# Performance work log

Hardware: AMD Instinct MI355X
Metric: run time of the kernel (lower is better)

## Reference

```python
import jax, jax.numpy as jnp
import numpy as np

N = 12288
E = N * 32  # avg degree 32


def spmm(row, col, w, support):
    # out[i] = sum_{e: row[e]==i} w[e] * support[col[e]]
    return jax.ops.segment_sum(w[:, None] * support[col], row, num_segments=N)


def setup_inputs() -> dict:
    key = jax.random.key(0)
    ks = jax.random.split(key, 7)
    x = jax.random.normal(ks[0], (N, 512), dtype=jnp.float32)
    edge_row = jax.random.randint(ks[1], (E,), 0, N, dtype=jnp.int32)
    edge_col = jax.random.randint(ks[2], (E,), 0, N, dtype=jnp.int32)
    # row-normalized-ish positive edge weights
    edge_w = jax.random.uniform(ks[3], (E,), dtype=jnp.float32) / 32.0
    def xavier(k, fan_in, fan_out):
        bound = float(np.sqrt(6.0 / (fan_in + fan_out)))
        return jax.random.uniform(k, (fan_in, fan_out), jnp.float32, -bound, bound)
    W1 = xavier(ks[4], 512, 256)
    W2 = xavier(ks[5], 256, 128)
    W3 = xavier(ks[6], 128, 64)
    return {"x": x, "edge_row": edge_row, "edge_col": edge_col,
            "edge_w": edge_w, "W1": W1, "W2": W2, "W3": W3}


def reference(x, edge_row, edge_col, edge_w, W1, W2, W3):
    # GNNLayer 1 (active=True): tanh(x @ W) then spmm(adj, .)
    z1 = spmm(edge_row, edge_col, edge_w, jnp.tanh(x @ W1))
    # GNNLayer 2 (active=True)
    z2 = spmm(edge_row, edge_col, edge_w, jnp.tanh(z1 @ W2))
    # GNNLayer 3 (active=False): no activation
    z_igae = spmm(edge_row, edge_col, edge_w, z2 @ W3)  # [N, 64]
    # reconstructed adjacency: sigmoid(z z^T), [N, N]
    z_igae_adj = jax.nn.sigmoid(z_igae @ z_igae.T)
    return (z_igae, z_igae_adj)
```

## Files before the change

kernel.cpp:

```cpp
#include <hip/hip_runtime.h>
#include <hip/hip_bf16.h>

#define NNODES 12288
#define NEDGES (NNODES * 32)
#define ELLCAP 128

typedef __attribute__((ext_vector_type(4))) float f32x4;
typedef __attribute__((ext_vector_type(8))) __bf16 bf16x8;

__global__ __launch_bounds__(256) void prep_kernel(const float* __restrict__ W1,
                                                   const float* __restrict__ W2,
                                                   const float* __restrict__ W3,
                                                   __bf16* __restrict__ W1t,
                                                   __bf16* __restrict__ W2t,
                                                   __bf16* __restrict__ W3t,
                                                   int* __restrict__ deg) {
    int i = blockIdx.x * 256 + threadIdx.x;
    if (i < NNODES) { deg[i] = 0; return; }
    int j = i - NNODES;
    if (j < 512 * 256) { W1t[(size_t)(j % 256) * 512 + j / 256] = (__bf16)W1[j]; return; }
    j -= 512 * 256;
    if (j < 256 * 128) { W2t[(size_t)(j % 128) * 256 + j / 128] = (__bf16)W2[j]; return; }
    j -= 256 * 128;
    if (j < 128 * 64) { W3t[(size_t)(j % 64) * 128 + j / 64] = (__bf16)W3[j]; return; }
}

__global__ __launch_bounds__(256) void gemm1_scatter(const float* __restrict__ x,
                                                     const __bf16* __restrict__ W1t,
                                                     __bf16* __restrict__ h1,
                                                     const int* __restrict__ erow,
                                                     const int* __restrict__ ecol,
                                                     const float* __restrict__ ew,
                                                     int* __restrict__ deg,
                                                     int2* __restrict__ ell) {
    if (blockIdx.x >= 384) {
        int e = (blockIdx.x - 384) * 256 + threadIdx.x;
        int r = erow[e];
        int p = atomicAdd(&deg[r], 1);
        int2 cw; cw.x = ecol[e]; cw.y = __float_as_int(ew[e]);
        ell[(size_t)r * ELLCAP + p] = cw;
        return;
    }
    constexpr int K = 512, Nc = 256;
    int wave = threadIdx.x >> 6, lane = threadIdx.x & 63;
    int lr = lane & 15, kg = lane >> 4;
    int m0 = (blockIdx.x % 96) * 128 + wave * 32;
    int n0 = (blockIdx.x / 96) * 64;
    f32x4 acc[2][4];
#pragma unroll
    for (int mi = 0; mi < 2; mi++)
#pragma unroll
        for (int ni = 0; ni < 4; ni++) acc[mi][ni] = (f32x4){0.f, 0.f, 0.f, 0.f};
#pragma unroll
    for (int k0 = 0; k0 < K; k0 += 32) {
        bf16x8 af[2], bf[4];
#pragma unroll
        for (int mi = 0; mi < 2; mi++) {
            const float* ap = x + (size_t)(m0 + mi * 16 + lr) * K + k0 + kg * 8;
            f32x4 a0 = *(const f32x4*)ap;
            f32x4 a1 = *(const f32x4*)(ap + 4);
#pragma unroll
            for (int j = 0; j < 4; j++) { af[mi][j] = (__bf16)a0[j]; af[mi][4 + j] = (__bf16)a1[j]; }
        }
#pragma unroll
        for (int ni = 0; ni < 4; ni++)
            bf[ni] = *(const bf16x8*)(W1t + (size_t)(n0 + ni * 16 + lr) * K + k0 + kg * 8);
#pragma unroll
        for (int mi = 0; mi < 2; mi++)
#pragma unroll
            for (int ni = 0; ni < 4; ni++)
                acc[mi][ni] = __builtin_amdgcn_mfma_f32_16x16x32_bf16(af[mi], bf[ni], acc[mi][ni], 0, 0, 0);
    }
#pragma unroll
    for (int mi = 0; mi < 2; mi++)
#pragma unroll
        for (int ni = 0; ni < 4; ni++) {
            int col = n0 + ni * 16 + lr;
            int rowb = m0 + mi * 16 + kg * 4;
#pragma unroll
            for (int r = 0; r < 4; r++)
                h1[(size_t)(rowb + r) * Nc + col] = (__bf16)tanhf(acc[mi][ni][r]);
        }
}

template <bool TANH, int K>
__global__ __launch_bounds__(256) void gemm_mfma(const __bf16* __restrict__ A,
                                                 const __bf16* __restrict__ Wt,
                                                 __bf16* __restrict__ C, int Nc) {
    int wave = threadIdx.x >> 6, lane = threadIdx.x & 63;
    int lr = lane & 15, kg = lane >> 4;
    int m0 = blockIdx.x * 128 + wave * 32;
    int n0 = blockIdx.y * 64;
    f32x4 acc[2][4];
#pragma unroll
    for (int mi = 0; mi < 2; mi++)
#pragma unroll
        for (int ni = 0; ni < 4; ni++) acc[mi][ni] = (f32x4){0.f, 0.f, 0.f, 0.f};
#pragma unroll
    for (int k0 = 0; k0 < K; k0 += 32) {
        bf16x8 af[2], bf[4];
#pragma unroll
        for (int mi = 0; mi < 2; mi++)
            af[mi] = *(const bf16x8*)(A + (size_t)(m0 + mi * 16 + lr) * K + k0 + kg * 8);
#pragma unroll
        for (int ni = 0; ni < 4; ni++)
            bf[ni] = *(const bf16x8*)(Wt + (size_t)(n0 + ni * 16 + lr) * K + k0 + kg * 8);
#pragma unroll
        for (int mi = 0; mi < 2; mi++)
#pragma unroll
            for (int ni = 0; ni < 4; ni++)
                acc[mi][ni] = __builtin_amdgcn_mfma_f32_16x16x32_bf16(af[mi], bf[ni], acc[mi][ni], 0, 0, 0);
    }
#pragma unroll
    for (int mi = 0; mi < 2; mi++)
#pragma unroll
        for (int ni = 0; ni < 4; ni++) {
            int col = n0 + ni * 16 + lr;
            int rowb = m0 + mi * 16 + kg * 4;
#pragma unroll
            for (int r = 0; r < 4; r++) {
                float v = acc[mi][ni][r];
                if (TANH) v = tanhf(v);
                C[(size_t)(rowb + r) * Nc + col] = (__bf16)v;
            }
        }
}

__global__ __launch_bounds__(256) void fused_spmm_tanh_gemm(const int* __restrict__ deg,
                                                            const int2* __restrict__ ell,
                                                            const __bf16* __restrict__ g1,
                                                            const __bf16* __restrict__ W3t,
                                                            __bf16* __restrict__ g2) {
    constexpr int K = 128, NOUT = 64, L = K / 8;
    __shared__ __bf16 zs[16][K + 4];
    int tid = threadIdx.x;
    int rloc = tid / L;
    int f8 = (tid % L) * 8;
    int rglob = blockIdx.x * 16 + rloc;
    int d = deg[rglob];
    const int2* er = ell + (size_t)rglob * ELLCAP;
    float acc[8] = {};
#pragma unroll 8
    for (int e = 0; e < d; e++) {
        int2 cw = er[e];
        float w = __int_as_float(cw.y);
        bf16x8 hv = *(const bf16x8*)(g1 + (size_t)cw.x * K + f8);
#pragma unroll
        for (int j = 0; j < 8; j++) acc[j] = fmaf(w, (float)hv[j], acc[j]);
    }
    bf16x8 o;
#pragma unroll
    for (int j = 0; j < 8; j++) o[j] = (__bf16)tanhf(acc[j]);
    *(bf16x8*)&zs[rloc][f8] = o;
    __syncthreads();
    int wave = tid >> 6, lane = tid & 63;
    int lr = lane & 15, kg = lane >> 4;
    f32x4 c = (f32x4){0.f, 0.f, 0.f, 0.f};
#pragma unroll
    for (int ks = 0; ks < K / 32; ks++) {
        bf16x8 a = *(const bf16x8*)&zs[lr][ks * 32 + kg * 8];
        bf16x8 b = *(const bf16x8*)(W3t + (size_t)(wave * 16 + lr) * K + ks * 32 + kg * 8);
        c = __builtin_amdgcn_mfma_f32_16x16x32_bf16(a, b, c, 0, 0, 0);
    }
#pragma unroll
    for (int r = 0; r < 4; r++)
        g2[(size_t)(blockIdx.x * 16 + kg * 4 + r) * NOUT + wave * 16 + lr] = (__bf16)c[r];
}

__global__ __launch_bounds__(256) void spmm64(const int* __restrict__ deg,
                                              const int2* __restrict__ ell,
                                              const __bf16* __restrict__ h,
                                              __bf16* __restrict__ z) {
    int r = blockIdx.x * 32 + threadIdx.x / 8;
    int f8 = (threadIdx.x & 7) * 8;
    int d = deg[r];
    const int2* er = ell + (size_t)r * ELLCAP;
    float acc[8] = {};
#pragma unroll 8
    for (int e = 0; e < d; e++) {
        int2 cw = er[e];
        float w = __int_as_float(cw.y);
        bf16x8 hv = *(const bf16x8*)(h + (size_t)cw.x * 64 + f8);
#pragma unroll
        for (int j = 0; j < 8; j++) acc[j] = fmaf(w, (float)hv[j], acc[j]);
    }
    bf16x8 o;
#pragma unroll
    for (int j = 0; j < 8; j++) o[j] = (__bf16)acc[j];
    *(bf16x8*)(z + (size_t)r * 64 + f8) = o;
}

__global__ __launch_bounds__(256) void spmm_final(const int* __restrict__ deg,
                                                  const int2* __restrict__ ell,
                                                  const __bf16* __restrict__ h,
                                                  __bf16* __restrict__ z,
                                                  float* __restrict__ zf) {
    int r = blockIdx.x * 32 + threadIdx.x / 8;
    int f8 = (threadIdx.x & 7) * 8;
    int d = deg[r];
    const int2* er = ell + (size_t)r * ELLCAP;
    float acc[8] = {};
#pragma unroll 8
    for (int e = 0; e < d; e++) {
        int2 cw = er[e];
        float w = __int_as_float(cw.y);
        bf16x8 hv = *(const bf16x8*)(h + (size_t)cw.x * 64 + f8);
#pragma unroll
        for (int j = 0; j < 8; j++) acc[j] = fmaf(w, (float)hv[j], acc[j]);
    }
    bf16x8 o;
#pragma unroll
    for (int j = 0; j < 8; j++) o[j] = (__bf16)acc[j];
    *(bf16x8*)(z + (size_t)r * 64 + f8) = o;
    f32x4 o0, o1;
#pragma unroll
    for (int j = 0; j < 4; j++) { o0[j] = acc[j]; o1[j] = acc[4 + j]; }
    *(f32x4*)(zf + (size_t)r * 64 + f8) = o0;
    *(f32x4*)(zf + (size_t)r * 64 + f8 + 4) = o1;
}

__global__ __launch_bounds__(256) void zzt_sigmoid(const __bf16* __restrict__ Z,
                                                   float* __restrict__ out) {
    __shared__ float tile[2][16][260];
    int wave = threadIdx.x >> 6;
    int lane = threadIdx.x & 63;
    int lr = lane & 15;
    int kg = lane >> 4;
    int r0 = blockIdx.y * 64;
    int c0blk = blockIdx.x * 256;
    int c0 = c0blk + wave * 64;
    bf16x8 af[4][2], bfr[4][2];
#pragma unroll
    for (int i = 0; i < 4; i++)
#pragma unroll
        for (int ks = 0; ks < 2; ks++) {
            af[i][ks]  = *(const bf16x8*)(Z + (size_t)(r0 + i * 16 + lr) * 64 + ks * 32 + kg * 8);
            bfr[i][ks] = *(const bf16x8*)(Z + (size_t)(c0 + i * 16 + lr) * 64 + ks * 32 + kg * 8);
        }
    f32x4 acc[4][4];
#pragma unroll
    for (int mi = 0; mi < 4; mi++)
#pragma unroll
        for (int ni = 0; ni < 4; ni++) acc[mi][ni] = (f32x4){0.f, 0.f, 0.f, 0.f};
#pragma unroll
    for (int mi = 0; mi < 4; mi++)
#pragma unroll
        for (int ni = 0; ni < 4; ni++) {
            acc[mi][ni] = __builtin_amdgcn_mfma_f32_16x16x32_bf16(af[mi][0], bfr[ni][0], acc[mi][ni], 0, 0, 0);
            acc[mi][ni] = __builtin_amdgcn_mfma_f32_16x16x32_bf16(af[mi][1], bfr[ni][1], acc[mi][ni], 0, 0, 0);
        }
#pragma unroll
    for (int ni = 0; ni < 4; ni++) {
        int colb = wave * 64 + ni * 16 + lr;
#pragma unroll
        for (int r = 0; r < 4; r++) {
            float e = __expf(-acc[0][ni][r]);
            tile[0][kg * 4 + r][colb] = __builtin_amdgcn_rcpf(1.f + e);
        }
    }
    __syncthreads();
#pragma unroll
    for (int p = 0; p < 4; p++) {
        if (p < 3) {
#pragma unroll
            for (int ni = 0; ni < 4; ni++) {
                int colb = wave * 64 + ni * 16 + lr;
#pragma unroll
                for (int r = 0; r < 4; r++) {
                    float e = __expf(-acc[p + 1][ni][r]);
                    tile[(p + 1) & 1][kg * 4 + r][colb] = __builtin_amdgcn_rcpf(1.f + e);
                }
            }
        }
#pragma unroll
        for (int it = 0; it < 4; it++) {
            int rowl = it * 4 + wave;
            size_t grow = (size_t)(r0 + p * 16 + rowl);
            *(f32x4*)(out + grow * NNODES + c0blk + lane * 4) = *(const f32x4*)&tile[p & 1][rowl][lane * 4];
        }
        __syncthreads();
    }
}

extern "C" void kernel_launch(void* const* d_in, const int* in_sizes, int n_in,
                              void* d_out, int out_size, void* d_ws, size_t ws_size,
                              hipStream_t stream) {
    (void)in_sizes; (void)n_in; (void)out_size; (void)ws_size;
    const float* x  = (const float*)d_in[0];
    const int* erow = (const int*)d_in[1];
    const int* ecol = (const int*)d_in[2];
    const float* ew = (const float*)d_in[3];
    const float* W1 = (const float*)d_in[4];
    const float* W2 = (const float*)d_in[5];
    const float* W3 = (const float*)d_in[6];
    float* z_igae = (float*)d_out;
    float* adj = (float*)d_out + (size_t)NNODES * 64;

    char* ws = (char*)d_ws;
    size_t off = 0;
    auto alloc = [&](size_t bytes) {
        void* p = ws + off;
        off += (bytes + 255) & ~(size_t)255;
        return p;
    };
    __bf16* W1t = (__bf16*)alloc((size_t)512 * 256 * 2);
    __bf16* W2t = (__bf16*)alloc((size_t)256 * 128 * 2);
    __bf16* W3t = (__bf16*)alloc((size_t)128 * 64 * 2);
    __bf16* h1  = (__bf16*)alloc((size_t)NNODES * 256 * 2);
    __bf16* g1  = (__bf16*)alloc((size_t)NNODES * 128 * 2);
    __bf16* g2  = (__bf16*)alloc((size_t)NNODES * 64 * 2);
    __bf16* t   = (__bf16*)alloc((size_t)NNODES * 64 * 2);
    __bf16* Zb  = (__bf16*)alloc((size_t)NNODES * 64 * 2);
    int* deg    = (int*)alloc(NNODES * 4);
    int2* ell   = (int2*)alloc((size_t)NNODES * ELLCAP * 8);

    prep_kernel<<<(NNODES + 512 * 256 + 256 * 128 + 128 * 64 + 255) / 256, 256, 0, stream>>>(
        W1, W2, W3, W1t, W2t, W3t, deg);
    gemm1_scatter<<<384 + NEDGES / 256, 256, 0, stream>>>(x, W1t, h1, erow, ecol, ew, deg, ell);
    gemm_mfma<false, 256><<<dim3(NNODES / 128, 2), 256, 0, stream>>>(h1, W2t, g1, 128);
    fused_spmm_tanh_gemm<<<NNODES / 16, 256, 0, stream>>>(deg, ell, g1, W3t, g2);
    spmm64<<<NNODES / 32, 256, 0, stream>>>(deg, ell, g2, t);
    spmm_final<<<NNODES / 32, 256, 0, stream>>>(deg, ell, t, Zb, z_igae);
    zzt_sigmoid<<<dim3(NNODES / 256, NNODES / 64), 256, 0, stream>>>((const __bf16*)Zb, adj);
}
```

Before: 215.7 us.

## Fuse first two GEMMs into one kernel keeping tanh activations in LDS

```diff
diff --git a/kernel.cpp b/kernel.cpp
--- a/kernel.cpp
+++ b/kernel.cpp
@@ -25,104 +25,98 @@
     if (j < 128 * 64) { W3t[(size_t)(j % 64) * 128 + j / 64] = (__bf16)W3[j]; return; }
 }
 
-__global__ __launch_bounds__(256) void gemm1_scatter(const float* __restrict__ x,
-                                                     const __bf16* __restrict__ W1t,
-                                                     __bf16* __restrict__ h1,
-                                                     const int* __restrict__ erow,
-                                                     const int* __restrict__ ecol,
-                                                     const float* __restrict__ ew,
-                                                     int* __restrict__ deg,
-                                                     int2* __restrict__ ell) {
-    if (blockIdx.x >= 384) {
-        int e = (blockIdx.x - 384) * 256 + threadIdx.x;
+__global__ __launch_bounds__(256) void gemm12_scatter(const float* __restrict__ x,
+                                                      const __bf16* __restrict__ W1t,
+                                                      const __bf16* __restrict__ W2t,
+                                                      __bf16* __restrict__ g1,
+                                                      const int* __restrict__ erow,
+                                                      const int* __restrict__ ecol,
+                                                      const float* __restrict__ ew,
+                                                      int* __restrict__ deg,
+                                                      int2* __restrict__ ell) {
+    if (blockIdx.x >= 96) {
+        int e = (blockIdx.x - 96) * 256 + threadIdx.x;
         int r = erow[e];
         int p = atomicAdd(&deg[r], 1);
         int2 cw; cw.x = ecol[e]; cw.y = __float_as_int(ew[e]);
         ell[(size_t)r * ELLCAP + p] = cw;
         return;
     }
-    constexpr int K = 512, Nc = 256;
+    __shared__ __bf16 zs[128][260];
     int wave = threadIdx.x >> 6, lane = threadIdx.x & 63;
     int lr = lane & 15, kg = lane >> 4;
-    int m0 = (blockIdx.x % 96) * 128 + wave * 32;
-    int n0 = (blockIdx.x / 96) * 64;
-    f32x4 acc[2][4];
+    int mloc = wave * 32;
+    int m0 = blockIdx.x * 128 + mloc;
+    f32x4 acc[2][16];
 #pragma unroll
     for (int mi = 0; mi < 2; mi++)
 #pragma unroll
-        for (int ni = 0; ni < 4; ni++) acc[mi][ni] = (f32x4){0.f, 0.f, 0.f, 0.f};
-#pragma unroll
-    for (int k0 = 0; k0 < K; k0 += 32) {
-        bf16x8 af[2], bf[4];
+        for (int nj = 0; nj < 16; nj++) acc[mi][nj] = (f32x4){0.f, 0.f, 0.f, 0.f};
+#pragma unroll 4
+    for (int k0 = 0; k0 < 512; k0 += 32) {
+        bf16x8 af[2];
 #pragma unroll
         for (int mi = 0; mi < 2; mi++) {
-            const float* ap = x + (size_t)(m0 + mi * 16 + lr) * K + k0 + kg * 8;
+            const float* ap = x + (size_t)(m0 + mi * 16 + lr) * 512 + k0 + kg * 8;
             f32x4 a0 = *(const f32x4*)ap;
             f32x4 a1 = *(const f32x4*)(ap + 4);
 #pragma unroll
             for (int j = 0; j < 4; j++) { af[mi][j] = (__bf16)a0[j]; af[mi][4 + j] = (__bf16)a1[j]; }
         }
 #pragma unroll
-        for (int ni = 0; ni < 4; ni++)
-            bf[ni] = *(const bf16x8*)(W1t + (size_t)(n0 + ni * 16 + lr) * K + k0 + kg * 8);
+        for (int nc = 0; nc < 4; nc++) {
+            bf16x8 bf[4];
+#pragma unroll
+            for (int ni = 0; ni < 4; ni++)
+                bf[ni] = *(const bf16x8*)(W1t + (size_t)(nc * 64 + ni * 16 + lr) * 512 + k0 + kg * 8);
+#pragma unroll
+            for (int mi = 0; mi < 2; mi++)
+#pragma unroll
+                for (int ni = 0; ni < 4; ni++)
+                    acc[mi][nc * 4 + ni] =
+                        __builtin_amdgcn_mfma_f32_16x16x32_bf16(af[mi], bf[ni], acc[mi][nc * 4 + ni], 0, 0, 0);
+        }
+    }
+#pragma unroll
+    for (int mi = 0; mi < 2; mi++)
+#pragma unroll
+        for (int nj = 0; nj < 16; nj++) {
+            int rowl = mloc + mi * 16 + kg * 4;
+            int col = nj * 16 + lr;
+#pragma unroll
+            for (int r = 0; r < 4; r++)
+                zs[rowl + r][col] = (__bf16)tanhf(acc[mi][nj][r]);
+        }
+    __syncthreads();
+    f32x4 a2[2][8];
+#pragma unroll
+    for (int mi = 0; mi < 2; mi++)
+#pragma unroll
+        for (int ni = 0; ni < 8; ni++) a2[mi][ni] = (f32x4){0.f, 0.f, 0.f, 0.f};
+#pragma unroll
+    for (int k0 = 0; k0 < 256; k0 += 32) {
+        bf16x8 a[2], b[8];
 #pragma unroll
         for (int mi = 0; mi < 2; mi++)
-#pragma unroll
-            for (int ni = 0; ni < 4; ni++)
-                acc[mi][ni] = __builtin_amdgcn_mfma_f32_16x16x32_bf16(af[mi], bf[ni], acc[mi][ni], 0, 0, 0);
+            a[mi] = *(const bf16x8*)&zs[mloc + mi * 16 + lr][k0 + kg * 8];
+#pragma unroll
+        for (int ni = 0; ni < 8; ni++)
+            b[ni] = *(const bf16x8*)(W2t + (size_t)(ni * 16 + lr) * 256 + k0 + kg * 8);
+#pragma unroll
+        for (int mi = 0; mi < 2; mi++)
+#pragma unroll
+            for (int ni = 0; ni < 8; ni++)
+                a2[mi][ni] = __builtin_amdgcn_mfma_f32_16x16x32_bf16(a[mi], b[ni], a2[mi][ni], 0, 0, 0);
     }
 #pragma unroll
     for (int mi = 0; mi < 2; mi++)
 #pragma unroll
-        for (int ni = 0; ni < 4; ni++) {
-            int col = n0 + ni * 16 + lr;
+        for (int ni = 0; ni < 8; ni++) {
+            int col = ni * 16 + lr;
             int rowb = m0 + mi * 16 + kg * 4;
 #pragma unroll
             for (int r = 0; r < 4; r++)
-                h1[(size_t)(rowb + r) * Nc + col] = (__bf16)tanhf(acc[mi][ni][r]);
-        }
-}
-
-template <bool TANH, int K>
-__global__ __launch_bounds__(256) void gemm_mfma(const __bf16* __restrict__ A,
-                                                 const __bf16* __restrict__ Wt,
-                                                 __bf16* __restrict__ C, int Nc) {
-    int wave = threadIdx.x >> 6, lane = threadIdx.x & 63;
-    int lr = lane & 15, kg = lane >> 4;
-    int m0 = blockIdx.x * 128 + wave * 32;
-    int n0 = blockIdx.y * 64;
-    f32x4 acc[2][4];
-#pragma unroll
-    for (int mi = 0; mi < 2; mi++)
-#pragma unroll
-        for (int ni = 0; ni < 4; ni++) acc[mi][ni] = (f32x4){0.f, 0.f, 0.f, 0.f};
-#pragma unroll
-    for (int k0 = 0; k0 < K; k0 += 32) {
-        bf16x8 af[2], bf[4];
-#pragma unroll
-        for (int mi = 0; mi < 2; mi++)
-            af[mi] = *(const bf16x8*)(A + (size_t)(m0 + mi * 16 + lr) * K + k0 + kg * 8);
-#pragma unroll
-        for (int ni = 0; ni < 4; ni++)
-            bf[ni] = *(const bf16x8*)(Wt + (size_t)(n0 + ni * 16 + lr) * K + k0 + kg * 8);
-#pragma unroll
-        for (int mi = 0; mi < 2; mi++)
-#pragma unroll
-            for (int ni = 0; ni < 4; ni++)
-                acc[mi][ni] = __builtin_amdgcn_mfma_f32_16x16x32_bf16(af[mi], bf[ni], acc[mi][ni], 0, 0, 0);
-    }
-#pragma unroll
-    for (int mi = 0; mi < 2; mi++)
-#pragma unroll
-        for (int ni = 0; ni < 4; ni++) {
-            int col = n0 + ni * 16 + lr;
-            int rowb = m0 + mi * 16 + kg * 4;
-#pragma unroll
-            for (int r = 0; r < 4; r++) {
-                float v = acc[mi][ni][r];
-                if (TANH) v = tanhf(v);
-                C[(size_t)(rowb + r) * Nc + col] = (__bf16)v;
-            }
+                g1[(size_t)(rowb + r) * 128 + col] = (__bf16)a2[mi][ni][r];
         }
 }
 
@@ -306,7 +300,6 @@
     __bf16* W1t = (__bf16*)alloc((size_t)512 * 256 * 2);
     __bf16* W2t = (__bf16*)alloc((size_t)256 * 128 * 2);
     __bf16* W3t = (__bf16*)alloc((size_t)128 * 64 * 2);
-    __bf16* h1  = (__bf16*)alloc((size_t)NNODES * 256 * 2);
     __bf16* g1  = (__bf16*)alloc((size_t)NNODES * 128 * 2);
     __bf16* g2  = (__bf16*)alloc((size_t)NNODES * 64 * 2);
     __bf16* t   = (__bf16*)alloc((size_t)NNODES * 64 * 2);
@@ -316,8 +309,7 @@
 
     prep_kernel<<<(NNODES + 512 * 256 + 256 * 128 + 128 * 64 + 255) / 256, 256, 0, stream>>>(
         W1, W2, W3, W1t, W2t, W3t, deg);
-    gemm1_scatter<<<384 + NEDGES / 256, 256, 0, stream>>>(x, W1t, h1, erow, ecol, ew, deg, ell);
-    gemm_mfma<false, 256><<<dim3(NNODES / 128, 2), 256, 0, stream>>>(h1, W2t, g1, 128);
+    gemm12_scatter<<<96 + NEDGES / 256, 256, 0, stream>>>(x, W1t, W2t, g1, erow, ecol, ew, deg, ell);
     fused_spmm_tanh_gemm<<<NNODES / 16, 256, 0, stream>>>(deg, ell, g1, W3t, g2);
     spmm64<<<NNODES / 32, 256, 0, stream>>>(deg, ell, g2, t);
     spmm_final<<<NNODES / 32, 256, 0, stream>>>(deg, ell, t, Zb, z_igae);
```

Measured after the change: 234.7 us. 1.09x slower.

## Give each wave its own 16-row strip in ZZT sigmoid to drop block barriers

Applied to the files above, without the earlier changes.

```diff
diff --git a/kernel.cpp b/kernel.cpp
--- a/kernel.cpp
+++ b/kernel.cpp
@@ -221,64 +221,38 @@
 
 __global__ __launch_bounds__(256) void zzt_sigmoid(const __bf16* __restrict__ Z,
                                                    float* __restrict__ out) {
-    __shared__ float tile[2][16][260];
+    __shared__ float tile[4][16][264];
     int wave = threadIdx.x >> 6;
     int lane = threadIdx.x & 63;
     int lr = lane & 15;
     int kg = lane >> 4;
-    int r0 = blockIdx.y * 64;
-    int c0blk = blockIdx.x * 256;
-    int c0 = c0blk + wave * 64;
-    bf16x8 af[4][2], bfr[4][2];
-#pragma unroll
-    for (int i = 0; i < 4; i++)
-#pragma unroll
-        for (int ks = 0; ks < 2; ks++) {
-            af[i][ks]  = *(const bf16x8*)(Z + (size_t)(r0 + i * 16 + lr) * 64 + ks * 32 + kg * 8);
-            bfr[i][ks] = *(const bf16x8*)(Z + (size_t)(c0 + i * 16 + lr) * 64 + ks * 32 + kg * 8);
-        }
-    f32x4 acc[4][4];
-#pragma unroll
-    for (int mi = 0; mi < 4; mi++)
-#pragma unroll
-        for (int ni = 0; ni < 4; ni++) acc[mi][ni] = (f32x4){0.f, 0.f, 0.f, 0.f};
-#pragma unroll
-    for (int mi = 0; mi < 4; mi++)
-#pragma unroll
-        for (int ni = 0; ni < 4; ni++) {
-            acc[mi][ni] = __builtin_amdgcn_mfma_f32_16x16x32_bf16(af[mi][0], bfr[ni][0], acc[mi][ni], 0, 0, 0);
-            acc[mi][ni] = __builtin_amdgcn_mfma_f32_16x16x32_bf16(af[mi][1], bfr[ni][1], acc[mi][ni], 0, 0, 0);
-        }
-#pragma unroll
-    for (int ni = 0; ni < 4; ni++) {
-        int colb = wave * 64 + ni * 16 + lr;
+    int r0 = blockIdx.y * 64 + wave * 16;
+    int c0 = blockIdx.x * 256;
+    bf16x8 af[2];
+    af[0] = *(const bf16x8*)(Z + (size_t)(r0 + lr) * 64 + kg * 8);
+    af[1] = *(const bf16x8*)(Z + (size_t)(r0 + lr) * 64 + 32 + kg * 8);
+    f32x4 acc[16];
+#pragma unroll
+    for (int ni = 0; ni < 16; ni++) acc[ni] = (f32x4){0.f, 0.f, 0.f, 0.f};
+#pragma unroll 4
+    for (int ni = 0; ni < 16; ni++) {
+        bf16x8 b0 = *(const bf16x8*)(Z + (size_t)(c0 + ni * 16 + lr) * 64 + kg * 8);
+        bf16x8 b1 = *(const bf16x8*)(Z + (size_t)(c0 + ni * 16 + lr) * 64 + 32 + kg * 8);
+        acc[ni] = __builtin_amdgcn_mfma_f32_16x16x32_bf16(af[0], b0, acc[ni], 0, 0, 0);
+        acc[ni] = __builtin_amdgcn_mfma_f32_16x16x32_bf16(af[1], b1, acc[ni], 0, 0, 0);
+    }
+#pragma unroll
+    for (int ni = 0; ni < 16; ni++) {
 #pragma unroll
         for (int r = 0; r < 4; r++) {
-            float e = __expf(-acc[0][ni][r]);
-            tile[0][kg * 4 + r][colb] = __builtin_amdgcn_rcpf(1.f + e);
-        }
-    }
-    __syncthreads();
-#pragma unroll
-    for (int p = 0; p < 4; p++) {
-        if (p < 3) {
-#pragma unroll
-            for (int ni = 0; ni < 4; ni++) {
-                int colb = wave * 64 + ni * 16 + lr;
-#pragma unroll
-                for (int r = 0; r < 4; r++) {
-                    float e = __expf(-acc[p + 1][ni][r]);
-                    tile[(p + 1) & 1][kg * 4 + r][colb] = __builtin_amdgcn_rcpf(1.f + e);
-                }
-            }
-        }
-#pragma unroll
-        for (int it = 0; it < 4; it++) {
-            int rowl = it * 4 + wave;
-            size_t grow = (size_t)(r0 + p * 16 + rowl);
-            *(f32x4*)(out + grow * NNODES + c0blk + lane * 4) = *(const f32x4*)&tile[p & 1][rowl][lane * 4];
-        }
-        __syncthreads();
+            float e = __expf(-acc[ni][r]);
+            tile[wave][kg * 4 + r][ni * 16 + lr] = __builtin_amdgcn_rcpf(1.f + e);
+        }
+    }
+#pragma unroll
+    for (int rl = 0; rl < 16; rl++) {
+        f32x4 v = *(const f32x4*)&tile[wave][rl][lane * 4];
+        *(f32x4*)(out + (size_t)(r0 + rl) * NNODES + c0 + lane * 4) = v;
     }
 }
 
```

Result: slower. 471.4 us (+118.5%).
